# Performance work log

Hardware: AMD Instinct MI355X
Metric: run time of the kernel (lower is better)

The kernel has to match this reference:

```python
import jax, jax.numpy as jnp
import numpy as np

DIM = 1024
CTX_DIM = 1024
HEADS = 16
HEAD_DIM = DIM // HEADS


def setup_inputs() -> dict:
    key = jax.random.key(0)
    ks = jax.random.split(key, 6)
    B, N, M = 2, 2048, 2048
    s = 0.02
    return {
        "x": jax.random.normal(ks[0], (B, N, DIM), dtype=jnp.float32),
        "context": jax.random.normal(ks[1], (B, M, CTX_DIM), dtype=jnp.float32),
        "W_q": jax.random.normal(ks[2], (DIM, DIM), dtype=jnp.float32) * s,
        "W_kv": jax.random.normal(ks[3], (CTX_DIM * 2, CTX_DIM), dtype=jnp.float32) * s,
        "W_proj": jax.random.normal(ks[4], (DIM, DIM), dtype=jnp.float32) * s,
        "b_proj": jax.random.normal(ks[5], (DIM,), dtype=jnp.float32) * s,
    }


def reference(x, context, W_q, W_kv, W_proj, b_proj):
    B, N, C = x.shape
    M = context.shape[1]
    scale = HEAD_DIM ** (-0.5)
    # q projection: [B,N,H,D]
    q = (x @ W_q.T).reshape(B, N, HEADS, HEAD_DIM) * scale
    # context kv projection: [B,M,2,H,D]
    kv = (context @ W_kv.T).reshape(B, M, 2, HEADS, HEAD_DIM)
    k = kv[:, :, 0]  # [B,M,H,D]
    v = kv[:, :, 0]  # NOTE: source uses qkv_context[0] for BOTH k and v (faithful)
    attn = jnp.einsum("bnhd,bmhd->bhnm", q, k)
    attn = jax.nn.softmax(attn, axis=-1)
    out = jnp.einsum("bhnm,bmhd->bnhd", attn, v).reshape(B, N, C)
    return out @ W_proj.T + b_proj
```

## Files before the change

### kernel.cpp

```cpp
#include <hip/hip_runtime.h>
#include <hip/hip_bf16.h>


typedef __bf16 bf16x8 __attribute__((ext_vector_type(8)));
typedef float f32x4 __attribute__((ext_vector_type(4)));

static constexpr int kDIM = 1024;
static constexpr float kLog2e = 1.4426950408889634f;

__device__ inline unsigned short f2bf(float f) {
    union { float f; unsigned int u; } v; v.f = f;
    return (unsigned short)((v.u + 0x7FFFu + ((v.u >> 16) & 1u)) >> 16);
}

__device__ inline void gload_lds16(const unsigned short* g, unsigned short* l) {
    __builtin_amdgcn_global_load_lds(
        (const __attribute__((address_space(1))) unsigned int*)g,
        (__attribute__((address_space(3))) unsigned int*)l, 16, 0, 0);
}

__global__ __launch_bounds__(256) void cast_all(
    const float* __restrict__ x, const float* __restrict__ ctx,
    const float* __restrict__ wq, const float* __restrict__ wkv,
    const float* __restrict__ wp,
    unsigned short* __restrict__ xb, unsigned short* __restrict__ cb,
    unsigned short* __restrict__ wqb, unsigned short* __restrict__ wkb,
    unsigned short* __restrict__ wpb)
{
    int j = blockIdx.x * 256 + threadIdx.x;
    const float* s; unsigned short* d;
    if (j < 1048576)                      { s = x;   d = xb;  }
    else if ((j -= 1048576) < 1048576)    { s = ctx; d = cb;  }
    else if ((j -= 1048576) < 262144)     { s = wq;  d = wqb; }
    else if ((j -= 262144) < 262144)      { s = wkv; d = wkb; }
    else if ((j -= 262144) < 262144)      { s = wp;  d = wpb; }
    else return;
    float4 f = ((const float4*)s)[j];
    ushort4 o;
    o.x = f2bf(f.x); o.y = f2bf(f.y); o.z = f2bf(f.z); o.w = f2bf(f.w);
    ((ushort4*)d)[j] = o;
}

__global__ __launch_bounds__(256) void gemm_qk(
    const unsigned short* __restrict__ xb, const unsigned short* __restrict__ cb,
    const unsigned short* __restrict__ Wq, const unsigned short* __restrict__ Wkv,
    unsigned short* __restrict__ Qb, unsigned short* __restrict__ Kb,
    unsigned short* __restrict__ Ktb, float qscale, int Mctx)
{
    __shared__ unsigned short As[128 * 64];
    __shared__ unsigned short Bs[128 * 64];
    const int z = blockIdx.z;
    const unsigned short* A  = z ? cb : xb;
    const unsigned short* Bw = z ? Wkv : Wq;
    unsigned short* Cb = z ? Kb : Qb;
    const float scale = z ? 1.0f : qscale;

    const int tid = threadIdx.x;
    const int wave = tid >> 6, lane = tid & 63;
    const int g = lane >> 4, c = lane & 15;
    const int wm = (wave & 1) * 64, wn = (wave >> 1) * 64;
    const int bm = blockIdx.y * 128, bn = blockIdx.x * 128;

    const int srow = lane >> 3, scol = (lane & 7) * 8;

    f32x4 acc[4][4];
    #pragma unroll
    for (int i = 0; i < 4; ++i)
        #pragma unroll
        for (int j = 0; j < 4; ++j)
            acc[i][j] = (f32x4){0.f, 0.f, 0.f, 0.f};

    for (int k0 = 0; k0 < kDIM; k0 += 64) {
        __syncthreads();
        #pragma unroll
        for (int t = 0; t < 4; ++t) {
            const int chunk = wave * 4 + t;
            const int row = chunk * 8 + srow;
            gload_lds16(A  + (size_t)(bm + row) * kDIM + k0 + scol, &As[chunk * 512]);
            gload_lds16(Bw + (size_t)(bn + row) * kDIM + k0 + scol, &Bs[chunk * 512]);
        }
        __syncthreads();
        #pragma unroll
        for (int kc = 0; kc < 2; ++kc) {
            bf16x8 af[4], bfr[4];
            #pragma unroll
            for (int i = 0; i < 4; ++i)
                af[i] = *(const bf16x8*)&As[(wm + i * 16 + c) * 64 + kc * 32 + g * 8];
            #pragma unroll
            for (int j = 0; j < 4; ++j)
                bfr[j] = *(const bf16x8*)&Bs[(wn + j * 16 + c) * 64 + kc * 32 + g * 8];
            #pragma unroll
            for (int i = 0; i < 4; ++i)
                #pragma unroll
                for (int j = 0; j < 4; ++j)
                    acc[i][j] = __builtin_amdgcn_mfma_f32_16x16x32_bf16(
                        af[i], bfr[j], acc[i][j], 0, 0, 0);
        }
    }

    #pragma unroll
    for (int i = 0; i < 4; ++i) {
        #pragma unroll
        for (int j = 0; j < 4; ++j) {
            const int r0 = bm + wm + i * 16 + 4 * g;
            const int cc = bn + wn + j * 16 + c;
            float v0 = acc[i][j][0] * scale;
            float v1 = acc[i][j][1] * scale;
            float v2 = acc[i][j][2] * scale;
            float v3 = acc[i][j][3] * scale;
            Cb[(size_t)(r0 + 0) * kDIM + cc] = f2bf(v0);
            Cb[(size_t)(r0 + 1) * kDIM + cc] = f2bf(v1);
            Cb[(size_t)(r0 + 2) * kDIM + cc] = f2bf(v2);
            Cb[(size_t)(r0 + 3) * kDIM + cc] = f2bf(v3);
            if (z) {
                const int bb = r0 / Mctx, n0 = r0 % Mctx;
                const int hh = cc >> 6, d = cc & 63;
                ushort4 pk;
                pk.x = f2bf(v0); pk.y = f2bf(v1); pk.z = f2bf(v2); pk.w = f2bf(v3);
                *(ushort4*)&Ktb[((size_t)((bb * 16 + hh) * 64 + d)) * Mctx + n0] = pk;
            }
        }
    }
}

__global__ __launch_bounds__(256) void gemm_proj(
    const unsigned short* __restrict__ Ab, const unsigned short* __restrict__ Wp,
    const float* __restrict__ bias, float* __restrict__ out)
{
    __shared__ unsigned short As[64 * 64];
    __shared__ unsigned short Bs[128 * 64];
    const int tid = threadIdx.x;
    const int wave = tid >> 6, lane = tid & 63;
    const int g = lane >> 4, c = lane & 15;
    const int wm = (wave & 1) * 32, wn = (wave >> 1) * 64;
    const int bm = blockIdx.y * 64, bn = blockIdx.x * 128;

    const int srow = lane >> 3, scol = (lane & 7) * 8;

    f32x4 acc[2][4];
    #pragma unroll
    for (int i = 0; i < 2; ++i)
        #pragma unroll
        for (int j = 0; j < 4; ++j)
            acc[i][j] = (f32x4){0.f, 0.f, 0.f, 0.f};

    for (int k0 = 0; k0 < kDIM; k0 += 64) {
        __syncthreads();
        #pragma unroll
        for (int t = 0; t < 2; ++t) {
            const int chunk = wave * 2 + t;
            const int row = chunk * 8 + srow;
            gload_lds16(Ab + (size_t)(bm + row) * kDIM + k0 + scol, &As[chunk * 512]);
        }
        #pragma unroll
        for (int t = 0; t < 4; ++t) {
            const int chunk = wave * 4 + t;
            const int row = chunk * 8 + srow;
            gload_lds16(Wp + (size_t)(bn + row) * kDIM + k0 + scol, &Bs[chunk * 512]);
        }
        __syncthreads();
        #pragma unroll
        for (int kc = 0; kc < 2; ++kc) {
            bf16x8 af[2], bfr[4];
            #pragma unroll
            for (int i = 0; i < 2; ++i)
                af[i] = *(const bf16x8*)&As[(wm + i * 16 + c) * 64 + kc * 32 + g * 8];
            #pragma unroll
            for (int j = 0; j < 4; ++j)
                bfr[j] = *(const bf16x8*)&Bs[(wn + j * 16 + c) * 64 + kc * 32 + g * 8];
            #pragma unroll
            for (int i = 0; i < 2; ++i)
                #pragma unroll
                for (int j = 0; j < 4; ++j)
                    acc[i][j] = __builtin_amdgcn_mfma_f32_16x16x32_bf16(
                        af[i], bfr[j], acc[i][j], 0, 0, 0);
        }
    }

    #pragma unroll
    for (int i = 0; i < 2; ++i) {
        #pragma unroll
        for (int j = 0; j < 4; ++j) {
            const int r0 = bm + wm + i * 16 + 4 * g;
            const int cc = bn + wn + j * 16 + c;
            const float bv = bias[cc];
            #pragma unroll
            for (int ii = 0; ii < 4; ++ii)
                out[(size_t)(r0 + ii) * kDIM + cc] = acc[i][j][ii] + bv;
        }
    }
}

__global__ __launch_bounds__(512) void attn_mfma_v4(
    const unsigned short* __restrict__ Q,
    const unsigned short* __restrict__ K,
    const unsigned short* __restrict__ Kt,
    unsigned short* __restrict__ O, int N, int M)
{
    __shared__ unsigned short Ks[64 * 72];
    __shared__ unsigned short Kts[64 * 72];
    __shared__ unsigned short Ps[128 * 72];

    const int b = blockIdx.z, h = blockIdx.y, q0 = blockIdx.x * 128;
    const int tid = threadIdx.x;
    const int wave = tid >> 6, lane = tid & 63;
    const int g = lane >> 4, c = lane & 15;

    const unsigned short* Qb = Q + (size_t)(b * N + q0 + wave * 16) * kDIM + h * 64;
    const unsigned short* Kb = K + (size_t)b * M * kDIM + h * 64;
    const unsigned short* Ktb = Kt + (size_t)((b * 16 + h) * 64) * M;
    unsigned short* Ob = O + (size_t)(b * N + q0) * kDIM + h * 64;

    bf16x8 aq[2];
    #pragma unroll
    for (int kc = 0; kc < 2; ++kc)
        aq[kc] = *(const bf16x8*)(Qb + (size_t)c * kDIM + kc * 32 + g * 8);

    f32x4 o[4];
    float l[4];
    #pragma unroll
    for (int dt = 0; dt < 4; ++dt) o[dt] = (f32x4){0.f, 0.f, 0.f, 0.f};
    #pragma unroll
    for (int ii = 0; ii < 4; ++ii) l[ii] = 0.0f;

    for (int k0 = 0; k0 < M; k0 += 64) {
        __syncthreads();
        {
            const int row = tid >> 3, col8 = (tid & 7) * 8;
            *(uint4*)&Ks[row * 72 + col8] =
                *(const uint4*)(Kb + (size_t)(k0 + row) * kDIM + col8);
            *(uint4*)&Kts[row * 72 + col8] =
                *(const uint4*)(Ktb + (size_t)row * M + k0 + col8);
        }
        __syncthreads();

        f32x4 s[4];
        #pragma unroll
        for (int nt = 0; nt < 4; ++nt) s[nt] = (f32x4){0.f, 0.f, 0.f, 0.f};
        #pragma unroll
        for (int kc = 0; kc < 2; ++kc) {
            #pragma unroll
            for (int nt = 0; nt < 4; ++nt) {
                bf16x8 bk = *(const bf16x8*)&Ks[(nt * 16 + c) * 72 + kc * 32 + g * 8];
                s[nt] = __builtin_amdgcn_mfma_f32_16x16x32_bf16(aq[kc], bk, s[nt], 0, 0, 0);
            }
        }

        #pragma unroll
        for (int nt = 0; nt < 4; ++nt)
            #pragma unroll
            for (int ii = 0; ii < 4; ++ii) {
                const float p = __builtin_amdgcn_exp2f(s[nt][ii]);
                l[ii] += p;
                Ps[(wave * 16 + 4 * g + ii) * 72 + nt * 16 + c] = f2bf(p);
            }

        #pragma unroll
        for (int nc = 0; nc < 2; ++nc) {
            bf16x8 pa = *(const bf16x8*)&Ps[(wave * 16 + c) * 72 + nc * 32 + g * 8];
            #pragma unroll
            for (int dt = 0; dt < 4; ++dt) {
                bf16x8 vb = *(const bf16x8*)&Kts[(dt * 16 + c) * 72 + nc * 32 + g * 8];
                o[dt] = __builtin_amdgcn_mfma_f32_16x16x32_bf16(pa, vb, o[dt], 0, 0, 0);
            }
        }
    }

    #pragma unroll
    for (int ii = 0; ii < 4; ++ii) {
        float sum = l[ii];
        #pragma unroll
        for (int mk = 1; mk < 16; mk <<= 1)
            sum += __shfl_xor(sum, mk);
        const float inv = 1.0f / sum;
        const int row = wave * 16 + 4 * g + ii;
        #pragma unroll
        for (int dt = 0; dt < 4; ++dt)
            Ob[(size_t)row * kDIM + dt * 16 + c] = f2bf(o[dt][ii] * inv);
    }
}

extern "C" void kernel_launch(void* const* d_in, const int* in_sizes, int n_in,
                              void* d_out, int out_size, void* d_ws, size_t ws_size,
                              hipStream_t stream)
{
    const float* x      = (const float*)d_in[0];
    const float* ctxp   = (const float*)d_in[1];
    const float* W_q    = (const float*)d_in[2];
    const float* W_kv   = (const float*)d_in[3];
    const float* W_proj = (const float*)d_in[4];
    const float* b_proj = (const float*)d_in[5];
    float* out = (float*)d_out;

    const int B = 2, N = 2048, M = 2048;
    const int BN = B * N;
    const int SQ = kDIM * kDIM;

    unsigned short* p = (unsigned short*)d_ws;
    unsigned short* xb  = p; p += (size_t)BN * kDIM;
    unsigned short* cb  = p; p += (size_t)BN * kDIM;
    unsigned short* wqb = p; p += SQ;
    unsigned short* wkb = p; p += SQ;
    unsigned short* wpb = p; p += SQ;
    unsigned short* Qb  = p; p += (size_t)BN * kDIM;
    unsigned short* Kb  = p; p += (size_t)BN * kDIM;
    unsigned short* Ktb = p; p += (size_t)BN * kDIM;
    unsigned short* Ab  = xb;

    hipLaunchKernelGGL(cast_all, dim3(11264), dim3(256), 0, stream,
                       x, ctxp, W_q, W_kv, W_proj, xb, cb, wqb, wkb, wpb);
    hipLaunchKernelGGL(gemm_qk, dim3(kDIM / 128, BN / 128, 2), dim3(256), 0, stream,
                       xb, cb, wqb, wkb, Qb, Kb, Ktb, 0.125f * kLog2e, M);
    hipLaunchKernelGGL(attn_mfma_v4, dim3(N / 128, 16, B), dim3(512), 0, stream,
                       Qb, Kb, Ktb, Ab, N, M);
    hipLaunchKernelGGL(gemm_proj, dim3(kDIM / 128, BN / 64), dim3(256), 0, stream,
                       Ab, wpb, b_proj, out);
}
```

Before: 212.6 us.

## Rewrite attention with 32x32 MFMA key-split and retile QK/proj GEMMs

The attention kernel now uses 32x32x16 MFMA tiles. Each pair of waves splits the 64-key block in half and computes S^T so that P can be packed to bf16 with a perm instruction. The two partial outputs are combined through shared memory at the end, and occupancy hints are raised with launch_bounds(512,4). The QK projection GEMM now uses 512 threads with smaller per-wave tiles, and the output projection GEMM uses 64x64 tiles to launch more blocks. These changes aim at better MFMA efficiency and occupancy, at the cost of an extra reduction pass and smaller reuse per wave in the GEMMs.

Result: faster. 195.6 us (-8.0%).

```diff
diff --git a/kernel.cpp b/kernel.cpp
--- a/kernel.cpp
+++ b/kernel.cpp
@@ -4,6 +4,7 @@
 
 typedef __bf16 bf16x8 __attribute__((ext_vector_type(8)));
 typedef float f32x4 __attribute__((ext_vector_type(4)));
+typedef float f32x16 __attribute__((ext_vector_type(16)));
 
 static constexpr int kDIM = 1024;
 static constexpr float kLog2e = 1.4426950408889634f;
@@ -11,6 +12,12 @@
 __device__ inline unsigned short f2bf(float f) {
     union { float f; unsigned int u; } v; v.f = f;
     return (unsigned short)((v.u + 0x7FFFu + ((v.u >> 16) & 1u)) >> 16);
+}
+
+__device__ inline unsigned int pack2bf(float a, float b) {
+    union { float f; unsigned int u; } ua, ub;
+    ua.f = a; ub.f = b;
+    return __builtin_amdgcn_perm(ub.u + 0x8000u, ua.u + 0x8000u, 0x07060302u);
 }
 
 __device__ inline void gload_lds16(const unsigned short* g, unsigned short* l) {
@@ -41,7 +48,7 @@
     ((ushort4*)d)[j] = o;
 }
 
-__global__ __launch_bounds__(256) void gemm_qk(
+__global__ __launch_bounds__(512) void gemm_qk(
     const unsigned short* __restrict__ xb, const unsigned short* __restrict__ cb,
     const unsigned short* __restrict__ Wq, const unsigned short* __restrict__ Wkv,
     unsigned short* __restrict__ Qb, unsigned short* __restrict__ Kb,
@@ -58,23 +65,23 @@
     const int tid = threadIdx.x;
     const int wave = tid >> 6, lane = tid & 63;
     const int g = lane >> 4, c = lane & 15;
-    const int wm = (wave & 1) * 64, wn = (wave >> 1) * 64;
+    const int wm = (wave & 1) * 64, wn = (wave >> 1) * 32;
     const int bm = blockIdx.y * 128, bn = blockIdx.x * 128;
 
     const int srow = lane >> 3, scol = (lane & 7) * 8;
 
-    f32x4 acc[4][4];
+    f32x4 acc[4][2];
     #pragma unroll
     for (int i = 0; i < 4; ++i)
         #pragma unroll
-        for (int j = 0; j < 4; ++j)
+        for (int j = 0; j < 2; ++j)
             acc[i][j] = (f32x4){0.f, 0.f, 0.f, 0.f};
 
     for (int k0 = 0; k0 < kDIM; k0 += 64) {
         __syncthreads();
         #pragma unroll
-        for (int t = 0; t < 4; ++t) {
-            const int chunk = wave * 4 + t;
+        for (int t = 0; t < 2; ++t) {
+            const int chunk = wave * 2 + t;
             const int row = chunk * 8 + srow;
             gload_lds16(A  + (size_t)(bm + row) * kDIM + k0 + scol, &As[chunk * 512]);
             gload_lds16(Bw + (size_t)(bn + row) * kDIM + k0 + scol, &Bs[chunk * 512]);
@@ -82,17 +89,17 @@
         __syncthreads();
         #pragma unroll
         for (int kc = 0; kc < 2; ++kc) {
-            bf16x8 af[4], bfr[4];
+            bf16x8 af[4], bfr[2];
             #pragma unroll
             for (int i = 0; i < 4; ++i)
                 af[i] = *(const bf16x8*)&As[(wm + i * 16 + c) * 64 + kc * 32 + g * 8];
             #pragma unroll
-            for (int j = 0; j < 4; ++j)
+            for (int j = 0; j < 2; ++j)
                 bfr[j] = *(const bf16x8*)&Bs[(wn + j * 16 + c) * 64 + kc * 32 + g * 8];
             #pragma unroll
             for (int i = 0; i < 4; ++i)
                 #pragma unroll
-                for (int j = 0; j < 4; ++j)
+                for (int j = 0; j < 2; ++j)
                     acc[i][j] = __builtin_amdgcn_mfma_f32_16x16x32_bf16(
                         af[i], bfr[j], acc[i][j], 0, 0, 0);
         }
@@ -101,7 +108,7 @@
     #pragma unroll
     for (int i = 0; i < 4; ++i) {
         #pragma unroll
-        for (int j = 0; j < 4; ++j) {
+        for (int j = 0; j < 2; ++j) {
             const int r0 = bm + wm + i * 16 + 4 * g;
             const int cc = bn + wn + j * 16 + c;
             float v0 = acc[i][j][0] * scale;
@@ -128,20 +135,20 @@
     const float* __restrict__ bias, float* __restrict__ out)
 {
     __shared__ unsigned short As[64 * 64];
-    __shared__ unsigned short Bs[128 * 64];
+    __shared__ unsigned short Bs[64 * 64];
     const int tid = threadIdx.x;
     const int wave = tid >> 6, lane = tid & 63;
     const int g = lane >> 4, c = lane & 15;
-    const int wm = (wave & 1) * 32, wn = (wave >> 1) * 64;
-    const int bm = blockIdx.y * 64, bn = blockIdx.x * 128;
+    const int wm = (wave & 1) * 32, wn = (wave >> 1) * 32;
+    const int bm = blockIdx.y * 64, bn = blockIdx.x * 64;
 
     const int srow = lane >> 3, scol = (lane & 7) * 8;
 
-    f32x4 acc[2][4];
+    f32x4 acc[2][2];
     #pragma unroll
     for (int i = 0; i < 2; ++i)
         #pragma unroll
-        for (int j = 0; j < 4; ++j)
+        for (int j = 0; j < 2; ++j)
             acc[i][j] = (f32x4){0.f, 0.f, 0.f, 0.f};
 
     for (int k0 = 0; k0 < kDIM; k0 += 64) {
@@ -151,27 +158,22 @@
             const int chunk = wave * 2 + t;
             const int row = chunk * 8 + srow;
             gload_lds16(Ab + (size_t)(bm + row) * kDIM + k0 + scol, &As[chunk * 512]);
-        }
-        #pragma unroll
-        for (int t = 0; t < 4; ++t) {
-            const int chunk = wave * 4 + t;
-            const int row = chunk * 8 + srow;
             gload_lds16(Wp + (size_t)(bn + row) * kDIM + k0 + scol, &Bs[chunk * 512]);
         }
         __syncthreads();
         #pragma unroll
         for (int kc = 0; kc < 2; ++kc) {
-            bf16x8 af[2], bfr[4];
+            bf16x8 af[2], bfr[2];
             #pragma unroll
             for (int i = 0; i < 2; ++i)
                 af[i] = *(const bf16x8*)&As[(wm + i * 16 + c) * 64 + kc * 32 + g * 8];
             #pragma unroll
-            for (int j = 0; j < 4; ++j)
+            for (int j = 0; j < 2; ++j)
                 bfr[j] = *(const bf16x8*)&Bs[(wn + j * 16 + c) * 64 + kc * 32 + g * 8];
             #pragma unroll
             for (int i = 0; i < 2; ++i)
                 #pragma unroll
-                for (int j = 0; j < 4; ++j)
+                for (int j = 0; j < 2; ++j)
                     acc[i][j] = __builtin_amdgcn_mfma_f32_16x16x32_bf16(
                         af[i], bfr[j], acc[i][j], 0, 0, 0);
         }
@@ -180,7 +182,7 @@
     #pragma unroll
     for (int i = 0; i < 2; ++i) {
         #pragma unroll
-        for (int j = 0; j < 4; ++j) {
+        for (int j = 0; j < 2; ++j) {
             const int r0 = bm + wm + i * 16 + 4 * g;
             const int cc = bn + wn + j * 16 + c;
             const float bv = bias[cc];
@@ -191,92 +193,115 @@
     }
 }
 
-__global__ __launch_bounds__(512) void attn_mfma_v4(
+__global__ __launch_bounds__(512, 4) void attn_mfma_v5(
     const unsigned short* __restrict__ Q,
     const unsigned short* __restrict__ K,
     const unsigned short* __restrict__ Kt,
     unsigned short* __restrict__ O, int N, int M)
 {
-    __shared__ unsigned short Ks[64 * 72];
-    __shared__ unsigned short Kts[64 * 72];
-    __shared__ unsigned short Ps[128 * 72];
+    __shared__ unsigned short smem[18432];
+    unsigned short* Ks  = smem;
+    unsigned short* Kts = smem + 64 * 72;
+    unsigned short* Ps  = smem + 2 * 64 * 72;
 
     const int b = blockIdx.z, h = blockIdx.y, q0 = blockIdx.x * 128;
     const int tid = threadIdx.x;
-    const int wave = tid >> 6, lane = tid & 63;
-    const int g = lane >> 4, c = lane & 15;
-
-    const unsigned short* Qb = Q + (size_t)(b * N + q0 + wave * 16) * kDIM + h * 64;
+    const int w = tid >> 6, lane = tid & 63;
+    const int strip = w >> 1, kh = w & 1;
+    const int ql = lane & 31, l5 = lane >> 5;
+
+    const unsigned short* Qrow = Q + (size_t)(b * N + q0 + strip * 32 + ql) * kDIM + h * 64;
     const unsigned short* Kb = K + (size_t)b * M * kDIM + h * 64;
     const unsigned short* Ktb = Kt + (size_t)((b * 16 + h) * 64) * M;
-    unsigned short* Ob = O + (size_t)(b * N + q0) * kDIM + h * 64;
-
-    bf16x8 aq[2];
-    #pragma unroll
-    for (int kc = 0; kc < 2; ++kc)
-        aq[kc] = *(const bf16x8*)(Qb + (size_t)c * kDIM + kc * 32 + g * 8);
-
-    f32x4 o[4];
-    float l[4];
-    #pragma unroll
-    for (int dt = 0; dt < 4; ++dt) o[dt] = (f32x4){0.f, 0.f, 0.f, 0.f};
-    #pragma unroll
-    for (int ii = 0; ii < 4; ++ii) l[ii] = 0.0f;
+
+    bf16x8 bq[4];
+    #pragma unroll
+    for (int kc = 0; kc < 4; ++kc)
+        bq[kc] = *(const bf16x8*)(Qrow + kc * 16 + l5 * 8);
+
+    f32x16 ot[2];
+    #pragma unroll
+    for (int dt = 0; dt < 2; ++dt)
+        #pragma unroll
+        for (int r = 0; r < 16; ++r) ot[dt][r] = 0.f;
+    float lac = 0.f;
+
+    const int srow = tid >> 3, scol = (tid & 7) * 8;
+    unsigned short* prow = &Ps[(strip * 32 + ql) * 72 + kh * 32];
 
     for (int k0 = 0; k0 < M; k0 += 64) {
         __syncthreads();
-        {
-            const int row = tid >> 3, col8 = (tid & 7) * 8;
-            *(uint4*)&Ks[row * 72 + col8] =
-                *(const uint4*)(Kb + (size_t)(k0 + row) * kDIM + col8);
-            *(uint4*)&Kts[row * 72 + col8] =
-                *(const uint4*)(Ktb + (size_t)row * M + k0 + col8);
-        }
-        __syncthreads();
-
-        f32x4 s[4];
-        #pragma unroll
-        for (int nt = 0; nt < 4; ++nt) s[nt] = (f32x4){0.f, 0.f, 0.f, 0.f};
-        #pragma unroll
-        for (int kc = 0; kc < 2; ++kc) {
-            #pragma unroll
-            for (int nt = 0; nt < 4; ++nt) {
-                bf16x8 bk = *(const bf16x8*)&Ks[(nt * 16 + c) * 72 + kc * 32 + g * 8];
-                s[nt] = __builtin_amdgcn_mfma_f32_16x16x32_bf16(aq[kc], bk, s[nt], 0, 0, 0);
+        *(uint4*)&Ks[srow * 72 + scol] =
+            *(const uint4*)(Kb + (size_t)(k0 + srow) * kDIM + scol);
+        *(uint4*)&Kts[srow * 72 + scol] =
+            *(const uint4*)(Ktb + (size_t)srow * M + k0 + scol);
+        __syncthreads();
+
+        f32x16 st;
+        #pragma unroll
+        for (int r = 0; r < 16; ++r) st[r] = 0.f;
+        #pragma unroll
+        for (int kc = 0; kc < 4; ++kc) {
+            bf16x8 ak = *(const bf16x8*)&Ks[(kh * 32 + ql) * 72 + kc * 16 + l5 * 8];
+            st = __builtin_amdgcn_mfma_f32_32x32x16_bf16(ak, bq[kc], st, 0, 0, 0);
+        }
+
+        float pr[16];
+        #pragma unroll
+        for (int r = 0; r < 16; ++r) {
+            pr[r] = __builtin_amdgcn_exp2f(st[r]);
+            lac += pr[r];
+        }
+        unsigned int dw[8];
+        #pragma unroll
+        for (int p = 0; p < 8; ++p) dw[p] = pack2bf(pr[2 * p], pr[2 * p + 1]);
+        #pragma unroll
+        for (int pp = 0; pp < 4; ++pp)
+            *(uint2*)&prow[8 * pp + 4 * l5] = make_uint2(dw[2 * pp], dw[2 * pp + 1]);
+
+        #pragma unroll
+        for (int kc2 = 0; kc2 < 2; ++kc2) {
+            bf16x8 bp = *(const bf16x8*)&prow[kc2 * 16 + l5 * 8];
+            #pragma unroll
+            for (int dt = 0; dt < 2; ++dt) {
+                bf16x8 av = *(const bf16x8*)&Kts[(dt * 32 + ql) * 72 + kh * 32 + kc2 * 16 + l5 * 8];
+                ot[dt] = __builtin_amdgcn_mfma_f32_32x32x16_bf16(av, bp, ot[dt], 0, 0, 0);
             }
         }
-
-        #pragma unroll
-        for (int nt = 0; nt < 4; ++nt)
-            #pragma unroll
-            for (int ii = 0; ii < 4; ++ii) {
-                const float p = __builtin_amdgcn_exp2f(s[nt][ii]);
-                l[ii] += p;
-                Ps[(wave * 16 + 4 * g + ii) * 72 + nt * 16 + c] = f2bf(p);
+    }
+
+    float lw = lac + __shfl_xor(lac, 32);
+    float* Om = (float*)smem;
+    float* Lm = Om + 128 * 68;
+    const int qi = strip * 32 + ql;
+
+    __syncthreads();
+    if (kh == 1) {
+        #pragma unroll
+        for (int dt = 0; dt < 2; ++dt)
+            #pragma unroll
+            for (int rr = 0; rr < 4; ++rr)
+                *(f32x4*)&Om[qi * 68 + dt * 32 + 8 * rr + 4 * l5] =
+                    (f32x4){ot[dt][4 * rr], ot[dt][4 * rr + 1],
+                            ot[dt][4 * rr + 2], ot[dt][4 * rr + 3]};
+        if (l5 == 0) Lm[qi] = lw;
+    }
+    __syncthreads();
+    if (kh == 0) {
+        const float inv = 1.0f / (lw + Lm[qi]);
+        unsigned short* Ob = O + (size_t)(b * N + q0 + qi) * kDIM + h * 64;
+        #pragma unroll
+        for (int dt = 0; dt < 2; ++dt)
+            #pragma unroll
+            for (int rr = 0; rr < 4; ++rr) {
+                f32x4 pv = *(const f32x4*)&Om[qi * 68 + dt * 32 + 8 * rr + 4 * l5];
+                ushort4 u;
+                u.x = f2bf((ot[dt][4 * rr]     + pv[0]) * inv);
+                u.y = f2bf((ot[dt][4 * rr + 1] + pv[1]) * inv);
+                u.z = f2bf((ot[dt][4 * rr + 2] + pv[2]) * inv);
+                u.w = f2bf((ot[dt][4 * rr + 3] + pv[3]) * inv);
+                *(ushort4*)(Ob + dt * 32 + 8 * rr + 4 * l5) = u;
             }
-
-        #pragma unroll
-        for (int nc = 0; nc < 2; ++nc) {
-            bf16x8 pa = *(const bf16x8*)&Ps[(wave * 16 + c) * 72 + nc * 32 + g * 8];
-            #pragma unroll
-            for (int dt = 0; dt < 4; ++dt) {
-                bf16x8 vb = *(const bf16x8*)&Kts[(dt * 16 + c) * 72 + nc * 32 + g * 8];
-                o[dt] = __builtin_amdgcn_mfma_f32_16x16x32_bf16(pa, vb, o[dt], 0, 0, 0);
-            }
-        }
-    }
-
-    #pragma unroll
-    for (int ii = 0; ii < 4; ++ii) {
-        float sum = l[ii];
-        #pragma unroll
-        for (int mk = 1; mk < 16; mk <<= 1)
-            sum += __shfl_xor(sum, mk);
-        const float inv = 1.0f / sum;
-        const int row = wave * 16 + 4 * g + ii;
-        #pragma unroll
-        for (int dt = 0; dt < 4; ++dt)
-            Ob[(size_t)row * kDIM + dt * 16 + c] = f2bf(o[dt][ii] * inv);
     }
 }
 
@@ -309,10 +334,10 @@
 
     hipLaunchKernelGGL(cast_all, dim3(11264), dim3(256), 0, stream,
                        x, ctxp, W_q, W_kv, W_proj, xb, cb, wqb, wkb, wpb);
-    hipLaunchKernelGGL(gemm_qk, dim3(kDIM / 128, BN / 128, 2), dim3(256), 0, stream,
+    hipLaunchKernelGGL(gemm_qk, dim3(kDIM / 128, BN / 128, 2), dim3(512), 0, stream,
                        xb, cb, wqb, wkb, Qb, Kb, Ktb, 0.125f * kLog2e, M);
-    hipLaunchKernelGGL(attn_mfma_v4, dim3(N / 128, 16, B), dim3(512), 0, stream,
+    hipLaunchKernelGGL(attn_mfma_v5, dim3(N / 128, 16, B), dim3(512), 0, stream,
                        Qb, Kb, Ktb, Ab, N, M);
-    hipLaunchKernelGGL(gemm_proj, dim3(kDIM / 128, BN / 64), dim3(256), 0, stream,
+    hipLaunchKernelGGL(gemm_proj, dim3(kDIM / 64, BN / 64), dim3(256), 0, stream,
                        Ab, wpb, b_proj, out);
 }
```
